# Kernel tuning notes

Hardware: AMD Instinct MI355X
Metric: run time of the kernel (lower is better)

## Reference

```python
import jax, jax.numpy as jnp
import numpy as np

N_Q = 8  # number of residual quantization levels


def setup_inputs() -> dict:
    key = jax.random.key(0)
    k1, k2 = jax.random.split(key)
    hidden_states = jax.random.normal(k1, (8192, 128), dtype=jnp.float32)
    codebooks = jax.random.normal(k2, (N_Q, 256, 128), dtype=jnp.float32)
    return {"hidden_states": hidden_states, "codebooks": codebooks}


def reference(hidden_states, codebooks):
    """Residual VQ encode: per level, nearest codebook entry by L2, subtract, accumulate.

    hidden_states: [N, D]; codebooks: [n_q, bins, D].
    Returns (codes [n_q, N] int, quantized [N, D]).
    """
    residual = hidden_states
    quantized = jnp.zeros_like(hidden_states)
    codes = []
    for i in range(N_Q):  # small fixed loop over structurally distinct levels
        codebook = codebooks[i]  # [bins, D]
        # squared L2 distance, same math as the original broadcasted form
        dist = jnp.sum((residual[:, None, :] - codebook[None, :, :]) ** 2, axis=-1)  # [N, bins]
        idx = jnp.argmin(dist, axis=-1)  # [N]
        chosen = codebook[idx]  # [N, D]
        quantized = quantized + chosen
        residual = residual - chosen
        codes.append(idx)
    return jnp.stack(codes, axis=0), quantized
```

## Files before the change

kernel.cpp:

```cpp
#include <hip/hip_runtime.h>

#define NQ 8
#define BINS 256
#define D 128
#define RPB 32
#define THREADS 512
#define RSTRIDE 132
#define FREG 520

typedef short s8v __attribute__((ext_vector_type(8)));
typedef float f4v __attribute__((ext_vector_type(4)));

static __device__ __forceinline__ unsigned short bf16_rtne(float x) {
    unsigned u = __float_as_uint(x);
    unsigned r = (u + 0x7fffu + ((u >> 16) & 1u)) >> 16;
    return (unsigned short)r;
}
static __device__ __forceinline__ float bf16_to_f(unsigned short h) {
    return __uint_as_float(((unsigned)h) << 16);
}
struct Split3 { short h, m, l; };
static __device__ __forceinline__ Split3 split3(float x) {
    Split3 s;
    unsigned short hb = bf16_rtne(x);
    float r1 = x - bf16_to_f(hb);
    unsigned short mb = bf16_rtne(r1);
    unsigned short lb = bf16_rtne(r1 - bf16_to_f(mb));
    s.h = (short)hb; s.m = (short)mb; s.l = (short)lb;
    return s;
}
static __device__ __forceinline__ unsigned long long shfl_xor_u64(unsigned long long v, int mask) {
    int lo = (int)(unsigned)(v & 0xffffffffull);
    int hi = (int)(unsigned)(v >> 32);
    lo = __shfl_xor(lo, mask, 64);
    hi = __shfl_xor(hi, mask, 64);
    return ((unsigned long long)(unsigned)hi << 32) | (unsigned)lo;
}
static __device__ __forceinline__ unsigned long long u64min(unsigned long long a, unsigned long long b) {
    return a < b ? a : b;
}

__global__ __launch_bounds__(256) void rvq_prep(
    const float* __restrict__ cb, short* __restrict__ cb_hi,
    short* __restrict__ cb_mid, short* __restrict__ cb_lo,
    float* __restrict__ c2)
{
    __shared__ float st[16 * RSTRIDE];
    const int L = blockIdx.x >> 4;
    const int o = blockIdx.x & 15;
    const int t = threadIdx.x;

    const float4* src = (const float4*)(cb + ((size_t)L * BINS + o * 16) * D);
    #pragma unroll
    for (int i = 0; i < 2; ++i) {
        int f4 = i * 256 + t;
        int row = f4 >> 5, c4 = f4 & 31;
        float4 v = src[f4];
        float* d = &st[row * RSTRIDE + c4 * 4];
        d[0] = v.x; d[1] = v.y; d[2] = v.z; d[3] = v.w;
    }
    __syncthreads();

    const int bin = t >> 4;
    const int kc  = t & 15;
    const float* p = &st[bin * RSTRIDE + kc * 8];
    s8v h8, m8, l8;
    float s = 0.f;
    #pragma unroll
    for (int j = 0; j < 8; ++j) {
        float x = p[j];
        Split3 sp = split3(x);
        h8[j] = sp.h; m8[j] = sp.m; l8[j] = sp.l;
        s = fmaf(x, x, s);
    }
    int idx = (L * 16 + kc) * BINS + (o * 16 + bin);
    ((s8v*)cb_hi)[idx]  = h8;
    ((s8v*)cb_mid)[idx] = m8;
    ((s8v*)cb_lo)[idx]  = l8;
    s += __shfl_xor(s, 1, 64);
    s += __shfl_xor(s, 2, 64);
    s += __shfl_xor(s, 4, 64);
    s += __shfl_xor(s, 8, 64);
    if (kc == 0) c2[L * BINS + o * 16 + bin] = s;
}

static __device__ __forceinline__ void frag_store(
    const float* rres, short* ah, short* am, short* al, int rr_, int g8)
{
    s8v h8, m8, l8;
    #pragma unroll
    for (int j = 0; j < 8; ++j) {
        Split3 sp = split3(rres[j]);
        h8[j] = sp.h; m8[j] = sp.m; l8[j] = sp.l;
    }
    int q = g8 & 3;
    int reg = (rr_ >> 4) * 4 + (g8 >> 2);
    int idx16 = q * 16 + (((rr_ & 15) + 4 * q) & 15);
    int off = reg * FREG + idx16 * 8;
    *(s8v*)&ah[off] = h8;
    *(s8v*)&am[off] = m8;
    *(s8v*)&al[off] = l8;
}

__global__ __launch_bounds__(THREADS, 2) void rvq_kernel(
    const float* __restrict__ hidden,
    const float* __restrict__ cb_f32,
    const short* __restrict__ cb_hi,
    const short* __restrict__ cb_mid,
    const short* __restrict__ cb_lo,
    const float* __restrict__ c2p,
    float* __restrict__ out_codes,
    float* __restrict__ out_quant,
    int N)
{
    __shared__ short ah[8 * FREG];
    __shared__ short am[8 * FREG];
    __shared__ short al[8 * FREG];
    __shared__ unsigned long long redw[RPB][8];

    const int t = threadIdx.x;
    const int w = t >> 6;
    const int l = t & 63;
    const int quad = l >> 4;
    const int m = l & 15;
    const int row0 = blockIdx.x * RPB;
    const int woff = w * 32;
    const int rr_ = t >> 4;
    const int g8 = t & 15;

    float rres[8];
    {
        const float4* hp = (const float4*)(hidden + (size_t)(row0 + rr_) * D + g8 * 8);
        float4 v0 = hp[0], v1 = hp[1];
        rres[0] = v0.x; rres[1] = v0.y; rres[2] = v0.z; rres[3] = v0.w;
        rres[4] = v1.x; rres[5] = v1.y; rres[6] = v1.z; rres[7] = v1.w;
    }
    frag_store(rres, ah, am, al, rr_, g8);

    const s8v* bhp = (const s8v*)cb_hi;
    const s8v* bmp = (const s8v*)cb_mid;
    const s8v* blp = (const s8v*)cb_lo;

    for (int level = 0; level < NQ; ++level) {
        s8v bh[2][4], bm[2][4], bl[2][4];
        float c2v[2];
        #pragma unroll
        for (int nt = 0; nt < 2; ++nt) {
            int bin = woff + nt * 16 + m;
            c2v[nt] = c2p[level * BINS + bin];
            #pragma unroll
            for (int ks = 0; ks < 4; ++ks) {
                int idx = (level * 16 + ks * 4 + quad) * BINS + bin;
                bh[nt][ks] = bhp[idx];
                bm[nt][ks] = bmp[idx];
                bl[nt][ks] = blp[idx];
            }
        }
        __syncthreads();

        s8v afh[2][4], afm[2][4], afl[2][4];
        #pragma unroll
        for (int mt = 0; mt < 2; ++mt)
            #pragma unroll
            for (int ks = 0; ks < 4; ++ks) {
                int idx16 = quad * 16 + ((m + 4 * quad) & 15);
                int off = (mt * 4 + ks) * FREG + idx16 * 8;
                afh[mt][ks] = *(const s8v*)&ah[off];
                afm[mt][ks] = *(const s8v*)&am[off];
                afl[mt][ks] = *(const s8v*)&al[off];
            }

        unsigned long long best[2][4];
        #pragma unroll
        for (int mt = 0; mt < 2; ++mt)
            #pragma unroll
            for (int i = 0; i < 4; ++i) best[mt][i] = ~0ull;

        #pragma unroll
        for (int nt = 0; nt < 2; ++nt) {
            const int bin = woff + nt * 16 + m;
            #pragma unroll
            for (int mt = 0; mt < 2; ++mt) {
                f4v a0 = {0.f, 0.f, 0.f, 0.f};
                f4v a1 = {0.f, 0.f, 0.f, 0.f};
                f4v a2 = {0.f, 0.f, 0.f, 0.f};
                #pragma unroll
                for (int ks = 0; ks < 4; ++ks) {
                    a0 = __builtin_amdgcn_mfma_f32_16x16x32_bf16(afh[mt][ks], bh[nt][ks], a0, 0, 0, 0);
                    a1 = __builtin_amdgcn_mfma_f32_16x16x32_bf16(afh[mt][ks], bm[nt][ks], a1, 0, 0, 0);
                    a1 = __builtin_amdgcn_mfma_f32_16x16x32_bf16(afm[mt][ks], bh[nt][ks], a1, 0, 0, 0);
                    a2 = __builtin_amdgcn_mfma_f32_16x16x32_bf16(afm[mt][ks], bm[nt][ks], a2, 0, 0, 0);
                    a2 = __builtin_amdgcn_mfma_f32_16x16x32_bf16(afh[mt][ks], bl[nt][ks], a2, 0, 0, 0);
                    a2 = __builtin_amdgcn_mfma_f32_16x16x32_bf16(afl[mt][ks], bh[nt][ks], a2, 0, 0, 0);
                }
                #pragma unroll
                for (int i = 0; i < 4; ++i) {
                    float dot = a0[i] + (a1[i] + a2[i]);
                    float k = fmaf(-2.f, dot, c2v[nt]);
                    unsigned u = __float_as_uint(k);
                    u = (u & 0x80000000u) ? ~u : (u | 0x80000000u);
                    unsigned long long key = ((unsigned long long)u << 32) | (unsigned)bin;
                    best[mt][i] = u64min(best[mt][i], key);
                }
            }
        }

        #pragma unroll
        for (int mt = 0; mt < 2; ++mt)
            #pragma unroll
            for (int i = 0; i < 4; ++i) {
                unsigned long long p = best[mt][i];
                p = u64min(p, shfl_xor_u64(p, 1));
                p = u64min(p, shfl_xor_u64(p, 2));
                p = u64min(p, shfl_xor_u64(p, 4));
                p = u64min(p, shfl_xor_u64(p, 8));
                if (m == 0) redw[mt * 16 + quad * 4 + i][w] = p;
            }
        __syncthreads();

        unsigned long long mn = redw[rr_][0];
        #pragma unroll
        for (int j = 1; j < 8; ++j) mn = u64min(mn, redw[rr_][j]);
        const int wb = (int)(mn & 0xffffffffull);
        if (g8 == 0)
            out_codes[(size_t)level * N + row0 + rr_] = (float)wb;

        {
            const float4* cp = (const float4*)(cb_f32 + ((size_t)level * BINS + wb) * D + g8 * 8);
            float4 c0 = cp[0], c1 = cp[1];
            rres[0] -= c0.x; rres[1] -= c0.y; rres[2] -= c0.z; rres[3] -= c0.w;
            rres[4] -= c1.x; rres[5] -= c1.y; rres[6] -= c1.z; rres[7] -= c1.w;
        }
        frag_store(rres, ah, am, al, rr_, g8);
    }

    {
        const float4* hp = (const float4*)(hidden + (size_t)(row0 + rr_) * D + g8 * 8);
        float4 v0 = hp[0], v1 = hp[1];
        float4 q0, q1;
        q0.x = v0.x - rres[0]; q0.y = v0.y - rres[1]; q0.z = v0.z - rres[2]; q0.w = v0.w - rres[3];
        q1.x = v1.x - rres[4]; q1.y = v1.y - rres[5]; q1.z = v1.z - rres[6]; q1.w = v1.w - rres[7];
        float4* op = (float4*)(out_quant + (size_t)(row0 + rr_) * D + g8 * 8);
        op[0] = q0; op[1] = q1;
    }
}

extern "C" void kernel_launch(void* const* d_in, const int* in_sizes, int n_in,
                              void* d_out, int out_size, void* d_ws, size_t ws_size,
                              hipStream_t stream) {
    const float* hidden    = (const float*)d_in[0];
    const float* codebooks = (const float*)d_in[1];
    float* out = (float*)d_out;
    const int N = in_sizes[0] / D;
    float* out_codes = out;
    float* out_quant = out + (size_t)NQ * N;

    char* ws = (char*)d_ws;
    short* cb_hi  = (short*)ws;
    short* cb_mid = (short*)(ws +  512 * 1024);
    short* cb_lo  = (short*)(ws + 1024 * 1024);
    float* c2     = (float*)(ws + 1536 * 1024);

    rvq_prep<<<dim3(NQ * 16), 256, 0, stream>>>(codebooks, cb_hi, cb_mid, cb_lo, c2);
    rvq_kernel<<<dim3(N / RPB), THREADS, 0, stream>>>(
        hidden, codebooks, cb_hi, cb_mid, cb_lo, c2, out_codes, out_quant, N);
}
```

Before: 110.9 us.

## Halve rows per block and stream codebook tiles with double-buffered prefetch

Blocks now cover 16 rows with 256 threads (4 waves). Each wave sweeps 64 bins as four 16-bin tiles, loading the next tile's bf16 split codebook fragments while the current tile's MFMAs run. This doubles the grid to 512 blocks for better CU coverage and lowers register pressure. The cost is that each codebook fragment now serves only 16 rows instead of 32, which doubles global or L2 codebook traffic per row.

```diff
diff --git a/kernel.cpp b/kernel.cpp
--- a/kernel.cpp
+++ b/kernel.cpp
@@ -3,8 +3,8 @@
 #define NQ 8
 #define BINS 256
 #define D 128
-#define RPB 32
-#define THREADS 512
+#define RPB 16
+#define THREADS 256
 #define RSTRIDE 132
 #define FREG 520
 
@@ -94,8 +94,8 @@
         h8[j] = sp.h; m8[j] = sp.m; l8[j] = sp.l;
     }
     int q = g8 & 3;
-    int reg = (rr_ >> 4) * 4 + (g8 >> 2);
-    int idx16 = q * 16 + (((rr_ & 15) + 4 * q) & 15);
+    int reg = g8 >> 2;
+    int idx16 = q * 16 + ((rr_ + 4 * q) & 15);
     int off = reg * FREG + idx16 * 8;
     *(s8v*)&ah[off] = h8;
     *(s8v*)&am[off] = m8;
@@ -113,10 +113,10 @@
     float* __restrict__ out_quant,
     int N)
 {
-    __shared__ short ah[8 * FREG];
-    __shared__ short am[8 * FREG];
-    __shared__ short al[8 * FREG];
-    __shared__ unsigned long long redw[RPB][8];
+    __shared__ short ah[4 * FREG];
+    __shared__ short am[4 * FREG];
+    __shared__ short al[4 * FREG];
+    __shared__ unsigned long long redw[RPB][4];
 
     const int t = threadIdx.x;
     const int w = t >> 6;
@@ -124,7 +124,7 @@
     const int quad = l >> 4;
     const int m = l & 15;
     const int row0 = blockIdx.x * RPB;
-    const int woff = w * 32;
+    const int woff = w * 64;
     const int rr_ = t >> 4;
     const int g8 = t & 15;
 
@@ -144,83 +144,84 @@
     for (int level = 0; level < NQ; ++level) {
         s8v bh[2][4], bm[2][4], bl[2][4];
         float c2v[2];
-        #pragma unroll
-        for (int nt = 0; nt < 2; ++nt) {
-            int bin = woff + nt * 16 + m;
-            c2v[nt] = c2p[level * BINS + bin];
+
+        {
+            int bin = woff + m;
+            c2v[0] = c2p[level * BINS + bin];
             #pragma unroll
             for (int ks = 0; ks < 4; ++ks) {
                 int idx = (level * 16 + ks * 4 + quad) * BINS + bin;
-                bh[nt][ks] = bhp[idx];
-                bm[nt][ks] = bmp[idx];
-                bl[nt][ks] = blp[idx];
+                bh[0][ks] = bhp[idx];
+                bm[0][ks] = bmp[idx];
+                bl[0][ks] = blp[idx];
             }
         }
         __syncthreads();
 
-        s8v afh[2][4], afm[2][4], afl[2][4];
-        #pragma unroll
-        for (int mt = 0; mt < 2; ++mt)
+        s8v afh[4], afm[4], afl[4];
+        #pragma unroll
+        for (int ks = 0; ks < 4; ++ks) {
+            int idx16 = quad * 16 + ((m + 4 * quad) & 15);
+            int off = ks * FREG + idx16 * 8;
+            afh[ks] = *(const s8v*)&ah[off];
+            afm[ks] = *(const s8v*)&am[off];
+            afl[ks] = *(const s8v*)&al[off];
+        }
+
+        unsigned long long best[4] = {~0ull, ~0ull, ~0ull, ~0ull};
+
+        #pragma unroll
+        for (int nt = 0; nt < 4; ++nt) {
+            const int cur = nt & 1;
+            if (nt < 3) {
+                int bin = woff + (nt + 1) * 16 + m;
+                c2v[1 - cur] = c2p[level * BINS + bin];
+                #pragma unroll
+                for (int ks = 0; ks < 4; ++ks) {
+                    int idx = (level * 16 + ks * 4 + quad) * BINS + bin;
+                    bh[1 - cur][ks] = bhp[idx];
+                    bm[1 - cur][ks] = bmp[idx];
+                    bl[1 - cur][ks] = blp[idx];
+                }
+            }
+            const int bin = woff + nt * 16 + m;
+            f4v a0 = {0.f, 0.f, 0.f, 0.f};
+            f4v a1 = {0.f, 0.f, 0.f, 0.f};
+            f4v a2 = {0.f, 0.f, 0.f, 0.f};
             #pragma unroll
             for (int ks = 0; ks < 4; ++ks) {
-                int idx16 = quad * 16 + ((m + 4 * quad) & 15);
-                int off = (mt * 4 + ks) * FREG + idx16 * 8;
-                afh[mt][ks] = *(const s8v*)&ah[off];
-                afm[mt][ks] = *(const s8v*)&am[off];
-                afl[mt][ks] = *(const s8v*)&al[off];
-            }
-
-        unsigned long long best[2][4];
-        #pragma unroll
-        for (int mt = 0; mt < 2; ++mt)
-            #pragma unroll
-            for (int i = 0; i < 4; ++i) best[mt][i] = ~0ull;
-
-        #pragma unroll
-        for (int nt = 0; nt < 2; ++nt) {
-            const int bin = woff + nt * 16 + m;
-            #pragma unroll
-            for (int mt = 0; mt < 2; ++mt) {
-                f4v a0 = {0.f, 0.f, 0.f, 0.f};
-                f4v a1 = {0.f, 0.f, 0.f, 0.f};
-                f4v a2 = {0.f, 0.f, 0.f, 0.f};
-                #pragma unroll
-                for (int ks = 0; ks < 4; ++ks) {
-                    a0 = __builtin_amdgcn_mfma_f32_16x16x32_bf16(afh[mt][ks], bh[nt][ks], a0, 0, 0, 0);
-                    a1 = __builtin_amdgcn_mfma_f32_16x16x32_bf16(afh[mt][ks], bm[nt][ks], a1, 0, 0, 0);
-                    a1 = __builtin_amdgcn_mfma_f32_16x16x32_bf16(afm[mt][ks], bh[nt][ks], a1, 0, 0, 0);
-                    a2 = __builtin_amdgcn_mfma_f32_16x16x32_bf16(afm[mt][ks], bm[nt][ks], a2, 0, 0, 0);
-                    a2 = __builtin_amdgcn_mfma_f32_16x16x32_bf16(afh[mt][ks], bl[nt][ks], a2, 0, 0, 0);
-                    a2 = __builtin_amdgcn_mfma_f32_16x16x32_bf16(afl[mt][ks], bh[nt][ks], a2, 0, 0, 0);
-                }
-                #pragma unroll
-                for (int i = 0; i < 4; ++i) {
-                    float dot = a0[i] + (a1[i] + a2[i]);
-                    float k = fmaf(-2.f, dot, c2v[nt]);
-                    unsigned u = __float_as_uint(k);
-                    u = (u & 0x80000000u) ? ~u : (u | 0x80000000u);
-                    unsigned long long key = ((unsigned long long)u << 32) | (unsigned)bin;
-                    best[mt][i] = u64min(best[mt][i], key);
-                }
-            }
-        }
-
-        #pragma unroll
-        for (int mt = 0; mt < 2; ++mt)
+                a0 = __builtin_amdgcn_mfma_f32_16x16x32_bf16(afh[ks], bh[cur][ks], a0, 0, 0, 0);
+                a1 = __builtin_amdgcn_mfma_f32_16x16x32_bf16(afh[ks], bm[cur][ks], a1, 0, 0, 0);
+                a1 = __builtin_amdgcn_mfma_f32_16x16x32_bf16(afm[ks], bh[cur][ks], a1, 0, 0, 0);
+                a2 = __builtin_amdgcn_mfma_f32_16x16x32_bf16(afm[ks], bm[cur][ks], a2, 0, 0, 0);
+                a2 = __builtin_amdgcn_mfma_f32_16x16x32_bf16(afh[ks], bl[cur][ks], a2, 0, 0, 0);
+                a2 = __builtin_amdgcn_mfma_f32_16x16x32_bf16(afl[ks], bh[cur][ks], a2, 0, 0, 0);
+            }
             #pragma unroll
             for (int i = 0; i < 4; ++i) {
-                unsigned long long p = best[mt][i];
-                p = u64min(p, shfl_xor_u64(p, 1));
-                p = u64min(p, shfl_xor_u64(p, 2));
-                p = u64min(p, shfl_xor_u64(p, 4));
-                p = u64min(p, shfl_xor_u64(p, 8));
-                if (m == 0) redw[mt * 16 + quad * 4 + i][w] = p;
-            }
+                float dot = a0[i] + (a1[i] + a2[i]);
+                float k = fmaf(-2.f, dot, c2v[cur]);
+                unsigned u = __float_as_uint(k);
+                u = (u & 0x80000000u) ? ~u : (u | 0x80000000u);
+                unsigned long long key = ((unsigned long long)u << 32) | (unsigned)bin;
+                best[i] = u64min(best[i], key);
+            }
+        }
+
+        #pragma unroll
+        for (int i = 0; i < 4; ++i) {
+            unsigned long long p = best[i];
+            p = u64min(p, shfl_xor_u64(p, 1));
+            p = u64min(p, shfl_xor_u64(p, 2));
+            p = u64min(p, shfl_xor_u64(p, 4));
+            p = u64min(p, shfl_xor_u64(p, 8));
+            if (m == 0) redw[quad * 4 + i][w] = p;
+        }
         __syncthreads();
 
         unsigned long long mn = redw[rr_][0];
         #pragma unroll
-        for (int j = 1; j < 8; ++j) mn = u64min(mn, redw[rr_][j]);
+        for (int j = 1; j < 4; ++j) mn = u64min(mn, redw[rr_][j]);
         const int wb = (int)(mn & 0xffffffffull);
         if (g8 == 0)
             out_codes[(size_t)level * N + row0 + rr_] = (float)wb;
```

After: 134.5 us. +21.3%, slower.

## Fuse codebook prep into main kernel via cooperative grid sync and prefetch next level

Applied to the files above, without the earlier changes.

Merges the codebook split/norm prep kernel into the main RVQ kernel. Each wave preps one codebook bin before a cooperative grid-wide sync, which removes the second kernel launch. Codebook fragments for the next level are now prefetched during the current level's reduction. The three MFMA accumulators are collapsed into one chain, which changes the summation order and lengthens the dependency chain. The cooperative launch requires all 256 blocks to be co-resident at 2 blocks per CU, and adds the cost of a grid barrier.

```diff
diff --git a/kernel.cpp b/kernel.cpp
--- a/kernel.cpp
+++ b/kernel.cpp
@@ -1,11 +1,13 @@
 #include <hip/hip_runtime.h>
+#include <hip/hip_cooperative_groups.h>
+
+namespace cg = cooperative_groups;
 
 #define NQ 8
 #define BINS 256
 #define D 128
 #define RPB 32
 #define THREADS 512
-#define RSTRIDE 132
 #define FREG 520
 
 typedef short s8v __attribute__((ext_vector_type(8)));
@@ -40,50 +42,6 @@
     return a < b ? a : b;
 }
 
-__global__ __launch_bounds__(256) void rvq_prep(
-    const float* __restrict__ cb, short* __restrict__ cb_hi,
-    short* __restrict__ cb_mid, short* __restrict__ cb_lo,
-    float* __restrict__ c2)
-{
-    __shared__ float st[16 * RSTRIDE];
-    const int L = blockIdx.x >> 4;
-    const int o = blockIdx.x & 15;
-    const int t = threadIdx.x;
-
-    const float4* src = (const float4*)(cb + ((size_t)L * BINS + o * 16) * D);
-    #pragma unroll
-    for (int i = 0; i < 2; ++i) {
-        int f4 = i * 256 + t;
-        int row = f4 >> 5, c4 = f4 & 31;
-        float4 v = src[f4];
-        float* d = &st[row * RSTRIDE + c4 * 4];
-        d[0] = v.x; d[1] = v.y; d[2] = v.z; d[3] = v.w;
-    }
-    __syncthreads();
-
-    const int bin = t >> 4;
-    const int kc  = t & 15;
-    const float* p = &st[bin * RSTRIDE + kc * 8];
-    s8v h8, m8, l8;
-    float s = 0.f;
-    #pragma unroll
-    for (int j = 0; j < 8; ++j) {
-        float x = p[j];
-        Split3 sp = split3(x);
-        h8[j] = sp.h; m8[j] = sp.m; l8[j] = sp.l;
-        s = fmaf(x, x, s);
-    }
-    int idx = (L * 16 + kc) * BINS + (o * 16 + bin);
-    ((s8v*)cb_hi)[idx]  = h8;
-    ((s8v*)cb_mid)[idx] = m8;
-    ((s8v*)cb_lo)[idx]  = l8;
-    s += __shfl_xor(s, 1, 64);
-    s += __shfl_xor(s, 2, 64);
-    s += __shfl_xor(s, 4, 64);
-    s += __shfl_xor(s, 8, 64);
-    if (kc == 0) c2[L * BINS + o * 16 + bin] = s;
-}
-
 static __device__ __forceinline__ void frag_store(
     const float* rres, short* ah, short* am, short* al, int rr_, int g8)
 {
@@ -102,13 +60,13 @@
     *(s8v*)&al[off] = l8;
 }
 
-__global__ __launch_bounds__(THREADS, 2) void rvq_kernel(
+__global__ __launch_bounds__(THREADS, 2) void rvq_fused(
     const float* __restrict__ hidden,
     const float* __restrict__ cb_f32,
-    const short* __restrict__ cb_hi,
-    const short* __restrict__ cb_mid,
-    const short* __restrict__ cb_lo,
-    const float* __restrict__ c2p,
+    short* __restrict__ cb_hi,
+    short* __restrict__ cb_mid,
+    short* __restrict__ cb_lo,
+    float* __restrict__ c2p,
     float* __restrict__ out_codes,
     float* __restrict__ out_quant,
     int N)
@@ -128,6 +86,39 @@
     const int rr_ = t >> 4;
     const int g8 = t & 15;
 
+    {
+        const int task = blockIdx.x * 8 + w;
+        const int L = task >> 8;
+        const int bin = task & 255;
+        if (l < 16) {
+            const float4* src = (const float4*)(cb_f32 + ((size_t)L * BINS + bin) * D) + l * 2;
+            float4 v0 = src[0], v1 = src[1];
+            float xs[8] = {v0.x, v0.y, v0.z, v0.w, v1.x, v1.y, v1.z, v1.w};
+            s8v h8, m8, l8;
+            float s = 0.f;
+            #pragma unroll
+            for (int j = 0; j < 8; ++j) {
+                Split3 sp = split3(xs[j]);
+                h8[j] = sp.h; m8[j] = sp.m; l8[j] = sp.l;
+                s = fmaf(xs[j], xs[j], s);
+            }
+            int idx = (L * 16 + l) * BINS + bin;
+            ((s8v*)cb_hi)[idx]  = h8;
+            ((s8v*)cb_mid)[idx] = m8;
+            ((s8v*)cb_lo)[idx]  = l8;
+            s += __shfl_xor(s, 1, 64);
+            s += __shfl_xor(s, 2, 64);
+            s += __shfl_xor(s, 4, 64);
+            s += __shfl_xor(s, 8, 64);
+            if (l == 0) c2p[L * BINS + bin] = s;
+        }
+    }
+    cg::this_grid().sync();
+
+    const s8v* bhp = (const s8v*)cb_hi;
+    const s8v* bmp = (const s8v*)cb_mid;
+    const s8v* blp = (const s8v*)cb_lo;
+
     float rres[8];
     {
         const float4* hp = (const float4*)(hidden + (size_t)(row0 + rr_) * D + g8 * 8);
@@ -137,33 +128,30 @@
     }
     frag_store(rres, ah, am, al, rr_, g8);
 
-    const s8v* bhp = (const s8v*)cb_hi;
-    const s8v* bmp = (const s8v*)cb_mid;
-    const s8v* blp = (const s8v*)cb_lo;
+    s8v bh[2][4], bm[2][4], bl[2][4];
+    float c2v[2];
+    #pragma unroll
+    for (int nt = 0; nt < 2; ++nt) {
+        int bin = woff + nt * 16 + m;
+        c2v[nt] = c2p[bin];
+        #pragma unroll
+        for (int ks = 0; ks < 4; ++ks) {
+            int idx = (ks * 4 + quad) * BINS + bin;
+            bh[nt][ks] = bhp[idx];
+            bm[nt][ks] = bmp[idx];
+            bl[nt][ks] = blp[idx];
+        }
+    }
 
     for (int level = 0; level < NQ; ++level) {
-        s8v bh[2][4], bm[2][4], bl[2][4];
-        float c2v[2];
-        #pragma unroll
-        for (int nt = 0; nt < 2; ++nt) {
-            int bin = woff + nt * 16 + m;
-            c2v[nt] = c2p[level * BINS + bin];
+        __syncthreads();
+
+        s8v afh[2][4], afm[2][4], afl[2][4];
+        const int idx16 = quad * 16 + ((m + 4 * quad) & 15);
+        #pragma unroll
+        for (int mt = 0; mt < 2; ++mt)
             #pragma unroll
             for (int ks = 0; ks < 4; ++ks) {
-                int idx = (level * 16 + ks * 4 + quad) * BINS + bin;
-                bh[nt][ks] = bhp[idx];
-                bm[nt][ks] = bmp[idx];
-                bl[nt][ks] = blp[idx];
-            }
-        }
-        __syncthreads();
-
-        s8v afh[2][4], afm[2][4], afl[2][4];
-        #pragma unroll
-        for (int mt = 0; mt < 2; ++mt)
-            #pragma unroll
-            for (int ks = 0; ks < 4; ++ks) {
-                int idx16 = quad * 16 + ((m + 4 * quad) & 15);
                 int off = (mt * 4 + ks) * FREG + idx16 * 8;
                 afh[mt][ks] = *(const s8v*)&ah[off];
                 afm[mt][ks] = *(const s8v*)&am[off];
@@ -182,21 +170,18 @@
             #pragma unroll
             for (int mt = 0; mt < 2; ++mt) {
                 f4v a0 = {0.f, 0.f, 0.f, 0.f};
-                f4v a1 = {0.f, 0.f, 0.f, 0.f};
-                f4v a2 = {0.f, 0.f, 0.f, 0.f};
                 #pragma unroll
                 for (int ks = 0; ks < 4; ++ks) {
                     a0 = __builtin_amdgcn_mfma_f32_16x16x32_bf16(afh[mt][ks], bh[nt][ks], a0, 0, 0, 0);
-                    a1 = __builtin_amdgcn_mfma_f32_16x16x32_bf16(afh[mt][ks], bm[nt][ks], a1, 0, 0, 0);
-                    a1 = __builtin_amdgcn_mfma_f32_16x16x32_bf16(afm[mt][ks], bh[nt][ks], a1, 0, 0, 0);
-                    a2 = __builtin_amdgcn_mfma_f32_16x16x32_bf16(afm[mt][ks], bm[nt][ks], a2, 0, 0, 0);
-                    a2 = __builtin_amdgcn_mfma_f32_16x16x32_bf16(afh[mt][ks], bl[nt][ks], a2, 0, 0, 0);
-                    a2 = __builtin_amdgcn_mfma_f32_16x16x32_bf16(afl[mt][ks], bh[nt][ks], a2, 0, 0, 0);
+                    a0 = __builtin_amdgcn_mfma_f32_16x16x32_bf16(afh[mt][ks], bm[nt][ks], a0, 0, 0, 0);
+                    a0 = __builtin_amdgcn_mfma_f32_16x16x32_bf16(afm[mt][ks], bh[nt][ks], a0, 0, 0, 0);
+                    a0 = __builtin_amdgcn_mfma_f32_16x16x32_bf16(afm[mt][ks], bm[nt][ks], a0, 0, 0, 0);
+                    a0 = __builtin_amdgcn_mfma_f32_16x16x32_bf16(afh[mt][ks], bl[nt][ks], a0, 0, 0, 0);
+                    a0 = __builtin_amdgcn_mfma_f32_16x16x32_bf16(afl[mt][ks], bh[nt][ks], a0, 0, 0, 0);
                 }
                 #pragma unroll
                 for (int i = 0; i < 4; ++i) {
-                    float dot = a0[i] + (a1[i] + a2[i]);
-                    float k = fmaf(-2.f, dot, c2v[nt]);
+                    float k = fmaf(-2.f, a0[i], c2v[nt]);
                     unsigned u = __float_as_uint(k);
                     u = (u & 0x80000000u) ? ~u : (u | 0x80000000u);
                     unsigned long long key = ((unsigned long long)u << 32) | (unsigned)bin;
@@ -216,6 +201,21 @@
                 p = u64min(p, shfl_xor_u64(p, 8));
                 if (m == 0) redw[mt * 16 + quad * 4 + i][w] = p;
             }
+
+        if (level + 1 < NQ) {
+            #pragma unroll
+            for (int nt = 0; nt < 2; ++nt) {
+                int bin = woff + nt * 16 + m;
+                c2v[nt] = c2p[(level + 1) * BINS + bin];
+                #pragma unroll
+                for (int ks = 0; ks < 4; ++ks) {
+                    int idx = ((level + 1) * 16 + ks * 4 + quad) * BINS + bin;
+                    bh[nt][ks] = bhp[idx];
+                    bm[nt][ks] = bmp[idx];
+                    bl[nt][ks] = blp[idx];
+                }
+            }
+        }
         __syncthreads();
 
         unsigned long long mn = redw[rr_][0];
@@ -251,7 +251,7 @@
     const float* hidden    = (const float*)d_in[0];
     const float* codebooks = (const float*)d_in[1];
     float* out = (float*)d_out;
-    const int N = in_sizes[0] / D;
+    int N = in_sizes[0] / D;
     float* out_codes = out;
     float* out_quant = out + (size_t)NQ * N;
 
@@ -261,7 +261,8 @@
     short* cb_lo  = (short*)(ws + 1024 * 1024);
     float* c2     = (float*)(ws + 1536 * 1024);
 
-    rvq_prep<<<dim3(NQ * 16), 256, 0, stream>>>(codebooks, cb_hi, cb_mid, cb_lo, c2);
-    rvq_kernel<<<dim3(N / RPB), THREADS, 0, stream>>>(
-        hidden, codebooks, cb_hi, cb_mid, cb_lo, c2, out_codes, out_quant, N);
-}
+    void* args[] = {(void*)&hidden, (void*)&codebooks, (void*)&cb_hi, (void*)&cb_mid,
+                    (void*)&cb_lo, (void*)&c2, (void*)&out_codes, (void*)&out_quant, (void*)&N};
+    hipLaunchCooperativeKernel((const void*)rvq_fused, dim3(N / RPB), dim3(THREADS),
+                               args, 0, stream);
+}
```

New measurement: 148.6 us. +34.0%, slower.

## Double block threads so each wave handles 16 bins and prefetch next-level codebook

Applied to the files above, without the earlier changes.

Raises the block to 1024 threads (16 waves), so each wave covers 16 codebook bins instead of 32 and each thread handles 4 residual elements instead of 8. The next level's codebook fragments are loaded before the barrier so they overlap with the cross-wave argmin reduction. The cross-wave reduction now merges 16 partials per row. This is meant to raise parallelism and hide global-load latency, at the cost of more barrier participants and a requested occupancy of 4 blocks per CU, which may pressure registers.

```diff
diff --git a/kernel.cpp b/kernel.cpp
--- a/kernel.cpp
+++ b/kernel.cpp
@@ -4,11 +4,12 @@
 #define BINS 256
 #define D 128
 #define RPB 32
-#define THREADS 512
+#define THREADS 1024
 #define RSTRIDE 132
 #define FREG 520
 
 typedef short s8v __attribute__((ext_vector_type(8)));
+typedef short s4v __attribute__((ext_vector_type(4)));
 typedef float f4v __attribute__((ext_vector_type(4)));
 
 static __device__ __forceinline__ unsigned short bf16_rtne(float x) {
@@ -84,25 +85,25 @@
     if (kc == 0) c2[L * BINS + o * 16 + bin] = s;
 }
 
-static __device__ __forceinline__ void frag_store(
-    const float* rres, short* ah, short* am, short* al, int rr_, int g8)
+static __device__ __forceinline__ void frag_store4(
+    const float* rres, short* ah, short* am, short* al, int rr_, int g8, int half)
 {
-    s8v h8, m8, l8;
+    s4v h4, m4, l4;
     #pragma unroll
-    for (int j = 0; j < 8; ++j) {
+    for (int j = 0; j < 4; ++j) {
         Split3 sp = split3(rres[j]);
-        h8[j] = sp.h; m8[j] = sp.m; l8[j] = sp.l;
+        h4[j] = sp.h; m4[j] = sp.m; l4[j] = sp.l;
     }
     int q = g8 & 3;
     int reg = (rr_ >> 4) * 4 + (g8 >> 2);
     int idx16 = q * 16 + (((rr_ & 15) + 4 * q) & 15);
-    int off = reg * FREG + idx16 * 8;
-    *(s8v*)&ah[off] = h8;
-    *(s8v*)&am[off] = m8;
-    *(s8v*)&al[off] = l8;
-}
-
-__global__ __launch_bounds__(THREADS, 2) void rvq_kernel(
+    int off = reg * FREG + idx16 * 8 + half * 4;
+    *(s4v*)&ah[off] = h4;
+    *(s4v*)&am[off] = m4;
+    *(s4v*)&al[off] = l4;
+}
+
+__global__ __launch_bounds__(THREADS, 4) void rvq_kernel(
     const float* __restrict__ hidden,
     const float* __restrict__ cb_f32,
     const short* __restrict__ cb_hi,
@@ -116,7 +117,7 @@
     __shared__ short ah[8 * FREG];
     __shared__ short am[8 * FREG];
     __shared__ short al[8 * FREG];
-    __shared__ unsigned long long redw[RPB][8];
+    __shared__ unsigned long long redw[RPB][16];
 
     const int t = threadIdx.x;
     const int w = t >> 6;
@@ -124,46 +125,48 @@
     const int quad = l >> 4;
     const int m = l & 15;
     const int row0 = blockIdx.x * RPB;
-    const int woff = w * 32;
-    const int rr_ = t >> 4;
-    const int g8 = t & 15;
-
-    float rres[8];
+    const int woff = w * 16;
+    const int rr_ = t >> 5;
+    const int g4 = t & 31;
+    const int g8 = g4 >> 1;
+    const int half = g4 & 1;
+
+    float rres[4];
     {
-        const float4* hp = (const float4*)(hidden + (size_t)(row0 + rr_) * D + g8 * 8);
-        float4 v0 = hp[0], v1 = hp[1];
-        rres[0] = v0.x; rres[1] = v0.y; rres[2] = v0.z; rres[3] = v0.w;
-        rres[4] = v1.x; rres[5] = v1.y; rres[6] = v1.z; rres[7] = v1.w;
-    }
-    frag_store(rres, ah, am, al, rr_, g8);
+        const float4* hp = (const float4*)(hidden + (size_t)(row0 + rr_) * D + g4 * 4);
+        float4 v = hp[0];
+        rres[0] = v.x; rres[1] = v.y; rres[2] = v.z; rres[3] = v.w;
+    }
+    frag_store4(rres, ah, am, al, rr_, g8, half);
 
     const s8v* bhp = (const s8v*)cb_hi;
     const s8v* bmp = (const s8v*)cb_mid;
     const s8v* blp = (const s8v*)cb_lo;
 
+    s8v bh[4], bm[4], bl[4];
+    float c2v;
+    {
+        int bin = woff + m;
+        c2v = c2p[bin];
+        #pragma unroll
+        for (int ks = 0; ks < 4; ++ks) {
+            int idx = (ks * 4 + quad) * BINS + bin;
+            bh[ks] = bhp[idx];
+            bm[ks] = bmp[idx];
+            bl[ks] = blp[idx];
+        }
+    }
+
     for (int level = 0; level < NQ; ++level) {
-        s8v bh[2][4], bm[2][4], bl[2][4];
-        float c2v[2];
-        #pragma unroll
-        for (int nt = 0; nt < 2; ++nt) {
-            int bin = woff + nt * 16 + m;
-            c2v[nt] = c2p[level * BINS + bin];
+        const int bin = woff + m;
+        __syncthreads();
+
+        s8v afh[2][4], afm[2][4], afl[2][4];
+        const int idx16 = quad * 16 + ((m + 4 * quad) & 15);
+        #pragma unroll
+        for (int mt = 0; mt < 2; ++mt)
             #pragma unroll
             for (int ks = 0; ks < 4; ++ks) {
-                int idx = (level * 16 + ks * 4 + quad) * BINS + bin;
-                bh[nt][ks] = bhp[idx];
-                bm[nt][ks] = bmp[idx];
-                bl[nt][ks] = blp[idx];
-            }
-        }
-        __syncthreads();
-
-        s8v afh[2][4], afm[2][4], afl[2][4];
-        #pragma unroll
-        for (int mt = 0; mt < 2; ++mt)
-            #pragma unroll
-            for (int ks = 0; ks < 4; ++ks) {
-                int idx16 = quad * 16 + ((m + 4 * quad) & 15);
                 int off = (mt * 4 + ks) * FREG + idx16 * 8;
                 afh[mt][ks] = *(const s8v*)&ah[off];
                 afm[mt][ks] = *(const s8v*)&am[off];
@@ -172,36 +175,26 @@
 
         unsigned long long best[2][4];
         #pragma unroll
-        for (int mt = 0; mt < 2; ++mt)
-            #pragma unroll
-            for (int i = 0; i < 4; ++i) best[mt][i] = ~0ull;
-
-        #pragma unroll
-        for (int nt = 0; nt < 2; ++nt) {
-            const int bin = woff + nt * 16 + m;
-            #pragma unroll
-            for (int mt = 0; mt < 2; ++mt) {
-                f4v a0 = {0.f, 0.f, 0.f, 0.f};
-                f4v a1 = {0.f, 0.f, 0.f, 0.f};
-                f4v a2 = {0.f, 0.f, 0.f, 0.f};
-                #pragma unroll
-                for (int ks = 0; ks < 4; ++ks) {
-                    a0 = __builtin_amdgcn_mfma_f32_16x16x32_bf16(afh[mt][ks], bh[nt][ks], a0, 0, 0, 0);
-                    a1 = __builtin_amdgcn_mfma_f32_16x16x32_bf16(afh[mt][ks], bm[nt][ks], a1, 0, 0, 0);
-                    a1 = __builtin_amdgcn_mfma_f32_16x16x32_bf16(afm[mt][ks], bh[nt][ks], a1, 0, 0, 0);
-                    a2 = __builtin_amdgcn_mfma_f32_16x16x32_bf16(afm[mt][ks], bm[nt][ks], a2, 0, 0, 0);
-                    a2 = __builtin_amdgcn_mfma_f32_16x16x32_bf16(afh[mt][ks], bl[nt][ks], a2, 0, 0, 0);
-                    a2 = __builtin_amdgcn_mfma_f32_16x16x32_bf16(afl[mt][ks], bh[nt][ks], a2, 0, 0, 0);
-                }
-                #pragma unroll
-                for (int i = 0; i < 4; ++i) {
-                    float dot = a0[i] + (a1[i] + a2[i]);
-                    float k = fmaf(-2.f, dot, c2v[nt]);
-                    unsigned u = __float_as_uint(k);
-                    u = (u & 0x80000000u) ? ~u : (u | 0x80000000u);
-                    unsigned long long key = ((unsigned long long)u << 32) | (unsigned)bin;
-                    best[mt][i] = u64min(best[mt][i], key);
-                }
+        for (int mt = 0; mt < 2; ++mt) {
+            f4v a0 = {0.f, 0.f, 0.f, 0.f};
+            f4v a1 = {0.f, 0.f, 0.f, 0.f};
+            f4v a2 = {0.f, 0.f, 0.f, 0.f};
+            #pragma unroll
+            for (int ks = 0; ks < 4; ++ks) {
+                a0 = __builtin_amdgcn_mfma_f32_16x16x32_bf16(afh[mt][ks], bh[ks], a0, 0, 0, 0);
+                a1 = __builtin_amdgcn_mfma_f32_16x16x32_bf16(afh[mt][ks], bm[ks], a1, 0, 0, 0);
+                a1 = __builtin_amdgcn_mfma_f32_16x16x32_bf16(afm[mt][ks], bh[ks], a1, 0, 0, 0);
+                a2 = __builtin_amdgcn_mfma_f32_16x16x32_bf16(afm[mt][ks], bm[ks], a2, 0, 0, 0);
+                a2 = __builtin_amdgcn_mfma_f32_16x16x32_bf16(afh[mt][ks], bl[ks], a2, 0, 0, 0);
+                a2 = __builtin_amdgcn_mfma_f32_16x16x32_bf16(afl[mt][ks], bh[ks], a2, 0, 0, 0);
+            }
+            #pragma unroll
+            for (int i = 0; i < 4; ++i) {
+                float dot = a0[i] + (a1[i] + a2[i]);
+                float k = fmaf(-2.f, dot, c2v);
+                unsigned u = __float_as_uint(k);
+                u = (u & 0x80000000u) ? ~u : (u | 0x80000000u);
+                best[mt][i] = ((unsigned long long)u << 32) | (unsigned)bin;
             }
         }
 
@@ -216,32 +209,41 @@
                 p = u64min(p, shfl_xor_u64(p, 8));
                 if (m == 0) redw[mt * 16 + quad * 4 + i][w] = p;
             }
+
+        if (level + 1 < NQ) {
+            c2v = c2p[(level + 1) * BINS + bin];
+            #pragma unroll
+            for (int ks = 0; ks < 4; ++ks) {
+                int idx = ((level + 1) * 16 + ks * 4 + quad) * BINS + bin;
+                bh[ks] = bhp[idx];
+                bm[ks] = bmp[idx];
+                bl[ks] = blp[idx];
+            }
+        }
         __syncthreads();
 
         unsigned long long mn = redw[rr_][0];
         #pragma unroll
-        for (int j = 1; j < 8; ++j) mn = u64min(mn, redw[rr_][j]);
+        for (int j = 1; j < 16; ++j) mn = u64min(mn, redw[rr_][j]);
         const int wb = (int)(mn & 0xffffffffull);
-        if (g8 == 0)
+        if (g4 == 0)
             out_codes[(size_t)level * N + row0 + rr_] = (float)wb;
 
         {
-            const float4* cp = (const float4*)(cb_f32 + ((size_t)level * BINS + wb) * D + g8 * 8);
-            float4 c0 = cp[0], c1 = cp[1];
-            rres[0] -= c0.x; rres[1] -= c0.y; rres[2] -= c0.z; rres[3] -= c0.w;
-            rres[4] -= c1.x; rres[5] -= c1.y; rres[6] -= c1.z; rres[7] -= c1.w;
-        }
-        frag_store(rres, ah, am, al, rr_, g8);
+            const float4* cp = (const float4*)(cb_f32 + ((size_t)level * BINS + wb) * D + g4 * 4);
+            float4 c = cp[0];
+            rres[0] -= c.x; rres[1] -= c.y; rres[2] -= c.z; rres[3] -= c.w;
+        }
+        frag_store4(rres, ah, am, al, rr_, g8, half);
     }
 
     {
-        const float4* hp = (const float4*)(hidden + (size_t)(row0 + rr_) * D + g8 * 8);
-        float4 v0 = hp[0], v1 = hp[1];
-        float4 q0, q1;
-        q0.x = v0.x - rres[0]; q0.y = v0.y - rres[1]; q0.z = v0.z - rres[2]; q0.w = v0.w - rres[3];
-        q1.x = v1.x - rres[4]; q1.y = v1.y - rres[5]; q1.z = v1.z - rres[6]; q1.w = v1.w - rres[7];
-        float4* op = (float4*)(out_quant + (size_t)(row0 + rr_) * D + g8 * 8);
-        op[0] = q0; op[1] = q1;
+        const float4* hp = (const float4*)(hidden + (size_t)(row0 + rr_) * D + g4 * 4);
+        float4 v = hp[0];
+        float4 q;
+        q.x = v.x - rres[0]; q.y = v.y - rres[1]; q.z = v.z - rres[2]; q.w = v.w - rres[3];
+        float4* op = (float4*)(out_quant + (size_t)(row0 + rr_) * D + g4 * 4);
+        op[0] = q;
     }
 }
 
```

Measured after the change: 113.9 us. 1.03x slower.
